# Kernel optimization log

Hardware: AMD Instinct MI355X
Metric: run time of the kernel (lower is better)

## Reference

```python
import jax, jax.numpy as jnp
import numpy as np

N, T, D, H = 128, 128, 1024, 1024


def setup_inputs() -> dict:
    key = jax.random.key(0)
    k_x, k_A, k_wx, k_wh, k_wa = jax.random.split(key, 5)
    x = jax.random.normal(k_x, (N, T, D), dtype=jnp.float32)
    A = jax.random.normal(k_A, (N, H, 4, 4), dtype=jnp.float32)
    Wx = jax.random.normal(k_wx, (D, 4 * H), dtype=jnp.float32) / np.sqrt(D)
    Wh = jax.random.normal(k_wh, (H, 4 * H), dtype=jnp.float32) / np.sqrt(H)
    Wattn = jax.random.normal(k_wa, (H, 4 * H), dtype=jnp.float32) / np.sqrt(H)
    b = jnp.zeros((4 * H,), dtype=jnp.float32)
    return {"x": x, "A": A, "Wx": Wx, "Wh": Wh, "Wattn": Wattn, "b": b}


def reference(x, A, Wx, Wh, Wattn, b):
    n, h_dim = A.shape[0], A.shape[1]
    A_flat = A.reshape(n, h_dim, 16)          # (N, H, 16) spatial flattened
    h0 = A_flat.mean(axis=-1)                 # meanpool over 4x4 grid
    c0 = h0
    scale = 1.0 / np.sqrt(h_dim).astype(np.float32)

    def step(carry, x_t):
        h, c = carry
        # scaled dot-product attention over 16 spatial cells
        attn_w = jax.nn.softmax(jnp.einsum('nh,nhk->nk', h, A_flat) * scale, axis=-1)
        attn = jnp.einsum('nhk,nk->nh', A_flat, attn_w)
        a = x_t @ Wx + h @ Wh + attn @ Wattn + b   # (N, 4H)
        a_i, a_f, a_o, a_g = jnp.split(a, 4, axis=1)
        c_next = jax.nn.sigmoid(a_f) * c + jax.nn.sigmoid(a_i) * jnp.tanh(a_g)
        h_next = jax.nn.sigmoid(a_o) * jnp.tanh(c_next)
        return (h_next, c_next), h_next

    xs = jnp.transpose(x, (1, 0, 2))          # (T, N, D)
    _, hs = jax.lax.scan(step, (h0, c0), xs)  # hs: (T, N, H)
    return jnp.transpose(hs, (1, 0, 2))       # (N, T, H)
```

## Files before the change

### kernel.cpp

```cpp
#include <hip/hip_runtime.h>
#include <math.h>

#define NB 128
#define TT 128
#define HD 1024
#define FH 4096
#define QB 16
#define QSLOT (QB * 2048)

typedef __attribute__((ext_vector_type(8))) short short8v;
typedef __attribute__((ext_vector_type(4))) float float4v;

__device__ __forceinline__ ushort f2b(float f) {
    union { float f; unsigned u; } v; v.f = f;
    unsigned r = (v.u + 0x7fffu + ((v.u >> 16) & 1u)) >> 16;
    return (ushort)r;
}
__device__ __forceinline__ float b2f(ushort u) {
    union { unsigned u; float f; } v; v.u = ((unsigned)u) << 16;
    return v.f;
}
__device__ __forceinline__ float sigm(float x) { return 1.f / (1.f + __expf(-x)); }
__device__ __forceinline__ void gll16(const void* g, void* l) {
    __builtin_amdgcn_global_load_lds(
        (const __attribute__((address_space(1))) void*)g,
        (__attribute__((address_space(3))) void*)l,
        16, 0, 0);
}
__device__ __forceinline__ int swz(int c, int r) {
    return (c & 8) | ((c & 7) ^ (r & 7));
}

__global__ __launch_bounds__(256) void cvt_x(const float* __restrict__ x,
                                             ushort* __restrict__ xb) {
    size_t i = (size_t)blockIdx.x * 256 + threadIdx.x;
    const float4* p = (const float4*)x + i * 2;
    float4 va = p[0], vb = p[1];
    union { ushort u[8]; uint4 v; } o;
    o.u[0] = f2b(va.x); o.u[1] = f2b(va.y); o.u[2] = f2b(va.z); o.u[3] = f2b(va.w);
    o.u[4] = f2b(vb.x); o.u[5] = f2b(vb.y); o.u[6] = f2b(vb.z); o.u[7] = f2b(vb.w);
    ((uint4*)xb)[i] = o.v;
}

__global__ __launch_bounds__(256) void build_wt(const float* __restrict__ Wx,
                                                const float* __restrict__ Wh,
                                                const float* __restrict__ Wattn,
                                                ushort* __restrict__ WT) {
    __shared__ ushort Ls[64][65];
    int k0 = blockIdx.x * 64, n0 = blockIdx.y * 64;
    const float* W; int m;
    if (k0 < 1024)      { W = Wx;    m = 0; }
    else if (k0 < 2048) { W = Wh;    m = 1; }
    else                { W = Wattn; m = 2; }
    const int kk0 = k0 - m * 1024;
    ushort* dstm = WT + (size_t)m * FH * 1024;
    int t = threadIdx.x;
    int cc = t & 63, r4 = t >> 6;
#pragma unroll
    for (int i = 0; i < 16; ++i) {
        int r = i * 4 + r4;
        Ls[r][cc] = f2b(W[(size_t)(kk0 + r) * FH + n0 + cc]);
    }
    __syncthreads();
#pragma unroll
    for (int i = 0; i < 16; ++i) {
        int nn = i * 4 + r4;
        dstm[(size_t)(n0 + nn) * 1024 + kk0 + cc] = Ls[cc][nn];
    }
}

__global__ __launch_bounds__(256) void init_kernel(
    const float* __restrict__ Aflat, float* __restrict__ cbuf,
    ushort* __restrict__ h0buf, ushort* __restrict__ Ab16,
    float* __restrict__ qk0, float* __restrict__ qk1)
{
    __shared__ float red[4][16];
    const int n = blockIdx.x, tid = threadIdx.x;
    const int wv = tid >> 6, l = tid & 63;
    float p[16];
#pragma unroll
    for (int k = 0; k < 16; ++k) p[k] = 0.f;
#pragma unroll
    for (int u = 0; u < 4; ++u) {
        const int h = tid + u * 256;
        const size_t idx = (size_t)n * 1024 + h;
        const float4* a4 = (const float4*)(Aflat + idx * 16);
        float ar[16];
#pragma unroll
        for (int q = 0; q < 4; ++q) {
            float4 v = a4[q];
            ar[q*4+0]=v.x; ar[q*4+1]=v.y; ar[q*4+2]=v.z; ar[q*4+3]=v.w;
        }
        union { ushort us[16]; uint4 v[2]; } ob;
#pragma unroll
        for (int k = 0; k < 16; ++k) ob.us[k] = f2b(ar[k]);
        uint4* dst = (uint4*)(Ab16 + idx * 16);
        dst[0] = ob.v[0]; dst[1] = ob.v[1];

        float s = 0.f;
#pragma unroll
        for (int k = 0; k < 16; ++k) s += ar[k];
        float hv = s * 0.0625f;
        cbuf[idx] = hv;
        h0buf[idx] = f2b(hv);
#pragma unroll
        for (int k = 0; k < 16; ++k) p[k] += hv * ar[k];
    }
#pragma unroll
    for (int k = 0; k < 16; ++k) {
        float v = p[k];
        v += __shfl_xor(v, 32); v += __shfl_xor(v, 16); v += __shfl_xor(v, 8);
        v += __shfl_xor(v, 4);  v += __shfl_xor(v, 2);  v += __shfl_xor(v, 1);
        p[k] = v;
    }
    if (l == 0) {
#pragma unroll
        for (int k = 0; k < 16; ++k) red[wv][k] = p[k];
    }
    __syncthreads();
    if (tid < 16) {
        float val = red[0][tid] + red[1][tid] + red[2][tid] + red[3][tid];
#pragma unroll
        for (int bkt = 0; bkt < QB; ++bkt) {
            qk0[bkt * 2048 + n * 16 + tid] = (bkt == 0) ? val : 0.f;
            qk1[bkt * 2048 + n * 16 + tid] = 0.f;
        }
    }
}

__global__ __launch_bounds__(256) void p_gemm(
    const ushort* __restrict__ Ab16,
    const ushort* __restrict__ WatT,
    ushort* __restrict__ P2)
{
    __shared__ ushort ALDS[4 * 16 * 72];
    __shared__ ushort Bs[256 * 64];
    const int tid = threadIdx.x;
    const int wv = tid >> 6, l = tid & 63;
    const int lr = l & 15, g = l >> 4;
    const int jt = blockIdx.x, n0 = blockIdx.y * 4;
    const int snn = tid >> 6, shl = tid & 63;

    float4v acc[4][4];
#pragma unroll
    for (int i = 0; i < 4; ++i)
#pragma unroll
        for (int j = 0; j < 4; ++j) acc[i][j] = (float4v){0.f, 0.f, 0.f, 0.f};

#pragma unroll 1
    for (int kc = 0; kc < 16; ++kc) {
        __syncthreads();
        {
            const ushort* src = Ab16 + ((size_t)(n0 + snn) * 1024 + kc * 64 + shl) * 16;
            union { uint4 v[2]; ushort us[16]; } iv;
            iv.v[0] = *(const uint4*)src;
            iv.v[1] = *(const uint4*)(src + 8);
#pragma unroll
            for (int k = 0; k < 16; ++k)
                ALDS[(snn * 16 + k) * 72 + shl] = iv.us[k];
        }
#pragma unroll
        for (int i = 0; i < 8; ++i) {
            int s = i * 256 + tid;
            int r = s >> 3, c = (s & 7) ^ (r & 7);
            gll16(WatT + (size_t)(jt * 256 + r) * 1024 + kc * 64 + c * 8,
                  &Bs[s * 8]);
        }
        __syncthreads();
#pragma unroll
        for (int sub = 0; sub < 2; ++sub) {
            short8v af[4], bf[4];
#pragma unroll
            for (int nn = 0; nn < 4; ++nn)
                af[nn] = *(const short8v*)&ALDS[(nn * 16 + lr) * 72 + sub * 32 + g * 8];
#pragma unroll
            for (int nf = 0; nf < 4; ++nf) {
                int rb = wv * 64 + nf * 16 + lr;
                bf[nf] = *(const short8v*)&Bs[rb * 64 + (((sub * 4 + g) ^ (rb & 7)) * 8)];
            }
#pragma unroll
            for (int nn = 0; nn < 4; ++nn)
#pragma unroll
                for (int nf = 0; nf < 4; ++nf)
                    acc[nn][nf] = __builtin_amdgcn_mfma_f32_16x16x32_bf16(
                        af[nn], bf[nf], acc[nn][nf], 0, 0, 0);
        }
    }

#pragma unroll
    for (int nn = 0; nn < 4; ++nn)
#pragma unroll
        for (int nf = 0; nf < 4; ++nf) {
            const int j = jt * 256 + wv * 64 + nf * 16 + lr;
            union { ushort u[4]; uint2 v; } o;
#pragma unroll
            for (int jj = 0; jj < 4; ++jj) o.u[jj] = f2b(acc[nn][nf][jj]);
            *(uint2*)&P2[((size_t)(n0 + nn) * FH + j) * 16 + g * 4] = o.v;
        }
}

__global__ __launch_bounds__(256) void step_kernel(
    const ushort* __restrict__ hcur,
    ushort* __restrict__ hnext,
    const ushort* __restrict__ xb_t,
    const ushort* __restrict__ WxT,
    const ushort* __restrict__ WhT,
    const ushort* __restrict__ P2,
    const ushort* __restrict__ Ab16,
    const float* __restrict__ bias,
    float* __restrict__ cbuf,
    const float* __restrict__ qk_cur,
    float* __restrict__ qk_next,
    float* __restrict__ qk_zero,
    float* __restrict__ out_t)
{
    __shared__ ushort AS[16384];
    __shared__ ushort BS[16384];
    __shared__ float accL[2 * 32 * 33];
    __shared__ float wLDS[32 * 16];

    const int tid = threadIdx.x;
    const int w = tid >> 6, l = tid & 63;
    const int mh = w & 1, kh = w >> 1;
    const int lr = l & 15, g = l >> 4;

    const int bid = blockIdx.x;
    const int xcd = bid & 7, ii = bid >> 3;
    const int bx = xcd * 16 + (ii & 15);
    const int my = ii >> 4;
    const int n0 = my * 32;

    if (bid < 128) qk_zero[bid * 256 + tid] = 0.f;

    if (tid < 32) {
        const float* q = qk_cur + (n0 + tid) * 16;
        float4 s4[4];
#pragma unroll
        for (int q4 = 0; q4 < 4; ++q4) s4[q4] = ((const float4*)q)[q4];
#pragma unroll
        for (int bkt = 1; bkt < QB; ++bkt) {
            const float4* qb = (const float4*)(q + bkt * 2048);
#pragma unroll
            for (int q4 = 0; q4 < 4; ++q4) {
                float4 v = qb[q4];
                s4[q4].x += v.x; s4[q4].y += v.y; s4[q4].z += v.z; s4[q4].w += v.w;
            }
        }
        float s[16];
#pragma unroll
        for (int q4 = 0; q4 < 4; ++q4) {
            s[q4*4+0] = s4[q4].x; s[q4*4+1] = s4[q4].y;
            s[q4*4+2] = s4[q4].z; s[q4*4+3] = s4[q4].w;
        }
        float m = -1e30f;
#pragma unroll
        for (int k = 0; k < 16; ++k) { s[k] *= 0.03125f; m = fmaxf(m, s[k]); }
        float sum = 0.f;
#pragma unroll
        for (int k = 0; k < 16; ++k) { s[k] = __expf(s[k] - m); sum += s[k]; }
        float inv = 1.f / sum;
#pragma unroll
        for (int k = 0; k < 16; ++k) wLDS[tid * 16 + k] = s[k] * inv;
    }

#define STAGE(b, kc)                                                           \
    do {                                                                       \
        _Pragma("unroll")                                                      \
        for (int i = 0; i < 4; ++i) {                                          \
            int u = i * 256 + tid;                                             \
            int skh = u >> 9, rem = u & 511;                                   \
            int r = rem >> 4, c = rem & 15;                                    \
            int lc = swz(c, r);                                                \
            const ushort* src = skh                                            \
                ? hcur + (size_t)(n0 + r) * 1024 + (kc) * 128 + lc * 8         \
                : xb_t + (size_t)(n0 + r) * (TT * HD) + (kc) * 128 + lc * 8;   \
            gll16(src, AS + (((b) * 2 + skh) * 512 + rem) * 8);                \
        }                                                                      \
        _Pragma("unroll")                                                      \
        for (int i = 0; i < 4; ++i) {                                          \
            int u = i * 256 + tid;                                             \
            int skh = u >> 9, rem = u & 511;                                   \
            int r = rem >> 4, c = rem & 15;                                    \
            int lc = swz(c, r);                                                \
            int jg = (r >> 3) * 1024 + bx * 8 + (r & 7);                       \
            const ushort* src = (skh ? WhT : WxT) + (size_t)jg * 1024          \
                                + (kc) * 128 + lc * 8;                         \
            gll16(src, BS + (((b) * 2 + skh) * 512 + rem) * 8);                \
        }                                                                      \
    } while (0)

    float4v acc[2];
    acc[0] = (float4v){0.f, 0.f, 0.f, 0.f};
    acc[1] = (float4v){0.f, 0.f, 0.f, 0.f};

    STAGE(0, 0);
    __syncthreads();
    int buf = 0;
#pragma unroll 1
    for (int kc = 0; kc < 8; ++kc) {
        if (kc < 7) STAGE(buf ^ 1, kc + 1);
        const int base = (buf * 2 + kh) * 512;
        const int ra = mh * 16 + lr;
#pragma unroll
        for (int ks = 0; ks < 4; ++ks) {
            const int c = ks * 4 + g;
            short8v af = *(const short8v*)&AS[(base + ra * 16 + swz(c, ra)) * 8];
#pragma unroll
            for (int nf = 0; nf < 2; ++nf) {
                const int rb = nf * 16 + lr;
                short8v bf = *(const short8v*)&BS[(base + rb * 16 + swz(c, rb)) * 8];
                acc[nf] = __builtin_amdgcn_mfma_f32_16x16x32_bf16(af, bf, acc[nf], 0, 0, 0);
            }
        }
        __syncthreads();
        buf ^= 1;
    }
#undef STAGE

#pragma unroll
    for (int nf = 0; nf < 2; ++nf)
#pragma unroll
        for (int jj = 0; jj < 4; ++jj)
            accL[(kh * 32 + mh * 16 + g * 4 + jj) * 33 + nf * 16 + lr] = acc[nf][jj];
    __syncthreads();

    const int n_l = tid >> 3, hcl = tid & 7;
    const int n = n0 + n_l;
    const int hc = bx * 8 + hcl;

    float wv_[16];
#pragma unroll
    for (int k = 0; k < 16; ++k) wv_[k] = wLDS[n_l * 16 + k];

    float val[4];
#pragma unroll
    for (int q = 0; q < 4; ++q) {
        const int cq = q * 8 + hcl;
        float v = accL[n_l * 33 + cq] + accL[(32 + n_l) * 33 + cq]
                + bias[q * 1024 + hc];
        const ushort* pp = P2 + ((size_t)n * FH + q * 1024 + hc) * 16;
        union { uint4 v[2]; ushort us[16]; } pv;
        pv.v[0] = *(const uint4*)pp;
        pv.v[1] = *(const uint4*)(pp + 8);
#pragma unroll
        for (int k = 0; k < 16; ++k) v += wv_[k] * b2f(pv.us[k]);
        val[q] = v;
    }

    const size_t chidx = (size_t)n * 1024 + hc;
    float cn = sigm(val[1]) * cbuf[chidx] + sigm(val[0]) * tanhf(val[3]);
    float hv = sigm(val[2]) * tanhf(cn);
    cbuf[chidx] = cn;
    out_t[(size_t)n * (TT * HD) + hc] = hv;
    hnext[chidx] = f2b(hv);

    union { uint4 v[2]; ushort us[16]; } av;
    {
        const ushort* ap = Ab16 + chidx * 16;
        av.v[0] = *(const uint4*)ap;
        av.v[1] = *(const uint4*)(ap + 8);
    }
    float vv[16];
#pragma unroll
    for (int k = 0; k < 16; ++k) vv[k] = hv * b2f(av.us[k]);
    {
        bool hi = (hcl & 1);
#pragma unroll
        for (int q = 0; q < 8; ++q) {
            float send = hi ? vv[q] : vv[q + 8];
            float recv = __shfl_xor(send, 1);
            vv[q] = (hi ? vv[q + 8] : vv[q]) + recv;
        }
        hi = (hcl & 2);
#pragma unroll
        for (int q = 0; q < 4; ++q) {
            float send = hi ? vv[q] : vv[q + 4];
            float recv = __shfl_xor(send, 2);
            vv[q] = (hi ? vv[q + 4] : vv[q]) + recv;
        }
        hi = (hcl & 4);
#pragma unroll
        for (int q = 0; q < 2; ++q) {
            float send = hi ? vv[q] : vv[q + 2];
            float recv = __shfl_xor(send, 4);
            vv[q] = (hi ? vv[q + 2] : vv[q]) + recv;
        }
    }
    const int kbase = ((hcl & 1) << 3) | ((hcl & 2) << 1) | ((hcl & 4) >> 1);
    float* qdst = qk_next + (bx & (QB - 1)) * 2048 + n * 16;
    atomicAdd(qdst + kbase,     vv[0]);
    atomicAdd(qdst + kbase + 1, vv[1]);
}

extern "C" void kernel_launch(void* const* d_in, const int* in_sizes, int n_in,
                              void* d_out, int out_size, void* d_ws, size_t ws_size,
                              hipStream_t stream) {
    const float* x     = (const float*)d_in[0];
    const float* A     = (const float*)d_in[1];
    const float* Wx    = (const float*)d_in[2];
    const float* Wh    = (const float*)d_in[3];
    const float* Wattn = (const float*)d_in[4];
    const float* b     = (const float*)d_in[5];
    float* out = (float*)d_out;

    ushort* WT   = (ushort*)d_ws;
    ushort* WxT  = WT;
    ushort* WhT  = WT + (size_t)FH * 1024;
    ushort* WatT = WT + (size_t)2 * FH * 1024;
    ushort* xb   = WT + (size_t)3 * FH * 1024;
    ushort* Ab16 = xb + (size_t)NB * TT * HD;
    ushort* hb   = Ab16 + (size_t)NB * HD * 16;
    float*  cb   = (float*)(hb + (size_t)2 * NB * HD);
    float*  qk   = cb + (size_t)NB * HD;
    ushort* P2   = (ushort*)(qk + 3 * QSLOT);

    cvt_x<<<8192, 256, 0, stream>>>(x, xb);
    build_wt<<<dim3(48, 64), 256, 0, stream>>>(Wx, Wh, Wattn, WT);
    init_kernel<<<NB, 256, 0, stream>>>(A, cb, hb, Ab16, qk, qk + QSLOT);
    p_gemm<<<dim3(16, 32), 256, 0, stream>>>(Ab16, WatT, P2);

    for (int t = 0; t < TT; ++t) {
        const ushort* hc = hb + (size_t)(t & 1) * NB * HD;
        ushort* hn       = hb + (size_t)((t + 1) & 1) * NB * HD;
        const float* qc  = qk + (size_t)(t % 3) * QSLOT;
        float* qn        = qk + (size_t)((t + 1) % 3) * QSLOT;
        float* qz        = qk + (size_t)((t + 2) % 3) * QSLOT;
        step_kernel<<<512, 256, 0, stream>>>(
            hc, hn, xb + (size_t)t * HD, WxT, WhT, P2, Ab16, b, cb,
            qc, qn, qz, out + (size_t)t * HD);
    }
}
```

Baseline: 2.046 ms.

## Precompute x@Wx for all timesteps in one batched GEMM before recurrence

Adds a large bf16 GEMM that computes the input projection x_t@Wx for every timestep up front and stores it in workspace. Each recurrent step kernel then only multiplies by Wh (half the K dimension) and adds the precomputed projection in the epilogue. This takes the x-projection off the sequential critical path and replaces the per-step Wx streaming with one efficient large GEMM. The cost is a 128MB workspace buffer and an extra bf16 rounding of the projection. A fallback path is kept for when the workspace is too small.

```diff
diff --git a/kernel.cpp b/kernel.cpp
--- a/kernel.cpp
+++ b/kernel.cpp
@@ -199,10 +199,109 @@
         }
 }
 
+__global__ __launch_bounds__(256) void xa_gemm2(
+    const float* __restrict__ x,
+    const ushort* __restrict__ WxT,
+    ushort* __restrict__ xab)
+{
+    __shared__ ushort As[2][128 * 64];
+    __shared__ ushort Bs[2][128 * 64];
+    const int tid = threadIdx.x;
+    const int w = tid >> 6, l = tid & 63;
+    const int wm = w >> 1, wn = w & 1;
+    const int lr = l & 15, g = l >> 4;
+    const int n0 = blockIdx.x * 128;
+    const int mt = blockIdx.y;
+    const float* Ax = x + (size_t)mt * 128 * 1024;
+    const ushort* Bb = WxT + (size_t)n0 * 1024;
+
+#define STAGEA(b, kf)                                                          \
+    do {                                                                       \
+        _Pragma("unroll")                                                      \
+        for (int i = 0; i < 4; ++i) {                                          \
+            int u = i * 256 + tid;                                             \
+            int r = u >> 3, c = u & 7;                                         \
+            const float* s = Ax + (size_t)r * 1024 + (kf) + c * 8;             \
+            float4 v0 = *(const float4*)s;                                     \
+            float4 v1 = *(const float4*)(s + 4);                               \
+            union { ushort us[8]; uint4 v; } o;                                \
+            o.us[0]=f2b(v0.x); o.us[1]=f2b(v0.y); o.us[2]=f2b(v0.z);           \
+            o.us[3]=f2b(v0.w); o.us[4]=f2b(v1.x); o.us[5]=f2b(v1.y);           \
+            o.us[6]=f2b(v1.z); o.us[7]=f2b(v1.w);                              \
+            *(uint4*)&As[b][(r * 8 + (c ^ (r & 7))) * 8] = o.v;                \
+        }                                                                      \
+    } while (0)
+#define STAGEB(b, kf)                                                          \
+    do {                                                                       \
+        _Pragma("unroll")                                                      \
+        for (int i = 0; i < 4; ++i) {                                          \
+            int s = i * 256 + tid;                                             \
+            int r = s >> 3, c = s & 7;                                         \
+            gll16(Bb + (size_t)r * 1024 + (kf) + (c ^ (r & 7)) * 8,            \
+                  &Bs[b][s * 8]);                                              \
+        }                                                                      \
+    } while (0)
+
+    float4v acc[4][4];
+#pragma unroll
+    for (int i = 0; i < 4; ++i)
+#pragma unroll
+        for (int j = 0; j < 4; ++j) acc[i][j] = (float4v){0.f, 0.f, 0.f, 0.f};
+
+    STAGEA(0, 0);
+    STAGEB(0, 0);
+    __syncthreads();
+    int buf = 0;
+#pragma unroll 1
+    for (int kc = 0; kc < 16; ++kc) {
+        if (kc < 15) { STAGEA(buf ^ 1, (kc + 1) * 64); STAGEB(buf ^ 1, (kc + 1) * 64); }
+        const ushort* Ab = As[buf];
+        const ushort* Bbuf = Bs[buf];
+#pragma unroll
+        for (int sub = 0; sub < 2; ++sub) {
+            short8v af[4], bf[4];
+#pragma unroll
+            for (int mf = 0; mf < 4; ++mf) {
+                int ra = wm * 64 + mf * 16 + lr;
+                af[mf] = *(const short8v*)&Ab[ra * 64 + (((sub * 4 + g) ^ (ra & 7)) * 8)];
+            }
+#pragma unroll
+            for (int nf = 0; nf < 4; ++nf) {
+                int rb = wn * 64 + nf * 16 + lr;
+                bf[nf] = *(const short8v*)&Bbuf[rb * 64 + (((sub * 4 + g) ^ (rb & 7)) * 8)];
+            }
+#pragma unroll
+            for (int mf = 0; mf < 4; ++mf)
+#pragma unroll
+                for (int nf = 0; nf < 4; ++nf)
+                    acc[mf][nf] = __builtin_amdgcn_mfma_f32_16x16x32_bf16(
+                        af[mf], bf[nf], acc[mf][nf], 0, 0, 0);
+        }
+        __syncthreads();
+        buf ^= 1;
+    }
+#undef STAGEA
+#undef STAGEB
+
+#pragma unroll
+    for (int mf = 0; mf < 4; ++mf)
+#pragma unroll
+        for (int nf = 0; nf < 4; ++nf) {
+            const int col = n0 + wn * 64 + nf * 16 + lr;
+#pragma unroll
+            for (int j = 0; j < 4; ++j) {
+                const int rl = wm * 64 + mf * 16 + g * 4 + j;
+                xab[((size_t)rl * NB + mt) * FH + col] = f2b(acc[mf][nf][j]);
+            }
+        }
+}
+
+template <int XAF>
 __global__ __launch_bounds__(256) void step_kernel(
     const ushort* __restrict__ hcur,
     ushort* __restrict__ hnext,
     const ushort* __restrict__ xb_t,
+    const ushort* __restrict__ xab_t,
     const ushort* __restrict__ WxT,
     const ushort* __restrict__ WhT,
     const ushort* __restrict__ P2,
@@ -271,9 +370,14 @@
             int skh = u >> 9, rem = u & 511;                                   \
             int r = rem >> 4, c = rem & 15;                                    \
             int lc = swz(c, r);                                                \
-            const ushort* src = skh                                            \
-                ? hcur + (size_t)(n0 + r) * 1024 + (kc) * 128 + lc * 8         \
-                : xb_t + (size_t)(n0 + r) * (TT * HD) + (kc) * 128 + lc * 8;   \
+            const ushort* src;                                                 \
+            if (XAF == 1)                                                      \
+                src = hcur + (size_t)(n0 + r) * 1024 + skh * 512               \
+                      + (kc) * 128 + lc * 8;                                   \
+            else                                                               \
+                src = skh                                                      \
+                    ? hcur + (size_t)(n0 + r) * 1024 + (kc) * 128 + lc * 8     \
+                    : xb_t + (size_t)(n0 + r) * (TT * HD) + (kc) * 128 + lc * 8;\
             gll16(src, AS + (((b) * 2 + skh) * 512 + rem) * 8);                \
         }                                                                      \
         _Pragma("unroll")                                                      \
@@ -283,8 +387,12 @@
             int r = rem >> 4, c = rem & 15;                                    \
             int lc = swz(c, r);                                                \
             int jg = (r >> 3) * 1024 + bx * 8 + (r & 7);                       \
-            const ushort* src = (skh ? WhT : WxT) + (size_t)jg * 1024          \
-                                + (kc) * 128 + lc * 8;                         \
+            const ushort* src;                                                 \
+            if (XAF == 1)                                                      \
+                src = WhT + (size_t)jg * 1024 + skh * 512 + (kc) * 128 + lc * 8;\
+            else                                                               \
+                src = (skh ? WhT : WxT) + (size_t)jg * 1024                    \
+                      + (kc) * 128 + lc * 8;                                   \
             gll16(src, BS + (((b) * 2 + skh) * 512 + rem) * 8);                \
         }                                                                      \
     } while (0)
@@ -293,12 +401,13 @@
     acc[0] = (float4v){0.f, 0.f, 0.f, 0.f};
     acc[1] = (float4v){0.f, 0.f, 0.f, 0.f};
 
+    const int NK = (XAF == 1) ? 4 : 8;
     STAGE(0, 0);
     __syncthreads();
     int buf = 0;
 #pragma unroll 1
-    for (int kc = 0; kc < 8; ++kc) {
-        if (kc < 7) STAGE(buf ^ 1, kc + 1);
+    for (int kc = 0; kc < NK; ++kc) {
+        if (kc + 1 < NK) STAGE(buf ^ 1, kc + 1);
         const int base = (buf * 2 + kh) * 512;
         const int ra = mh * 16 + lr;
 #pragma unroll
@@ -338,6 +447,7 @@
         const int cq = q * 8 + hcl;
         float v = accL[n_l * 33 + cq] + accL[(32 + n_l) * 33 + cq]
                 + bias[q * 1024 + hc];
+        if (XAF == 1) v += b2f(xab_t[(size_t)n * FH + q * 1024 + hc]);
         const ushort* pp = P2 + ((size_t)n * FH + q * 1024 + hc) * 16;
         union { uint4 v[2]; ushort us[16]; } pv;
         pv.v[0] = *(const uint4*)pp;
@@ -407,26 +517,46 @@
     ushort* WxT  = WT;
     ushort* WhT  = WT + (size_t)FH * 1024;
     ushort* WatT = WT + (size_t)2 * FH * 1024;
-    ushort* xb   = WT + (size_t)3 * FH * 1024;
-    ushort* Ab16 = xb + (size_t)NB * TT * HD;
+    ushort* Ab16 = WT + (size_t)3 * FH * 1024;
     ushort* hb   = Ab16 + (size_t)NB * HD * 16;
     float*  cb   = (float*)(hb + (size_t)2 * NB * HD);
     float*  qk   = cb + (size_t)NB * HD;
     ushort* P2   = (ushort*)(qk + 3 * QSLOT);
-
-    cvt_x<<<8192, 256, 0, stream>>>(x, xb);
+    ushort* tail = P2 + (size_t)NB * FH * 16;
+
+    const size_t base  = (size_t)((char*)tail - (char*)d_ws);
+    const size_t xasz  = (size_t)TT * NB * FH * 2;
+    const size_t xbsz  = (size_t)NB * TT * HD * 2;
+
     build_wt<<<dim3(48, 64), 256, 0, stream>>>(Wx, Wh, Wattn, WT);
     init_kernel<<<NB, 256, 0, stream>>>(A, cb, hb, Ab16, qk, qk + QSLOT);
     p_gemm<<<dim3(16, 32), 256, 0, stream>>>(Ab16, WatT, P2);
 
-    for (int t = 0; t < TT; ++t) {
-        const ushort* hc = hb + (size_t)(t & 1) * NB * HD;
-        ushort* hn       = hb + (size_t)((t + 1) & 1) * NB * HD;
-        const float* qc  = qk + (size_t)(t % 3) * QSLOT;
-        float* qn        = qk + (size_t)((t + 1) % 3) * QSLOT;
-        float* qz        = qk + (size_t)((t + 2) % 3) * QSLOT;
-        step_kernel<<<512, 256, 0, stream>>>(
-            hc, hn, xb + (size_t)t * HD, WxT, WhT, P2, Ab16, b, cb,
-            qc, qn, qz, out + (size_t)t * HD);
-    }
-}
+    if (ws_size >= base + xasz) {
+        ushort* xab = tail;
+        xa_gemm2<<<dim3(32, 128), 256, 0, stream>>>(x, WxT, xab);
+        for (int t = 0; t < TT; ++t) {
+            const ushort* hc = hb + (size_t)(t & 1) * NB * HD;
+            ushort* hn       = hb + (size_t)((t + 1) & 1) * NB * HD;
+            const float* qc  = qk + (size_t)(t % 3) * QSLOT;
+            float* qn        = qk + (size_t)((t + 1) % 3) * QSLOT;
+            float* qz        = qk + (size_t)((t + 2) % 3) * QSLOT;
+            step_kernel<1><<<512, 256, 0, stream>>>(
+                hc, hn, nullptr, xab + (size_t)t * NB * FH, WxT, WhT, P2, Ab16,
+                b, cb, qc, qn, qz, out + (size_t)t * HD);
+        }
+    } else {
+        ushort* xb = tail;
+        cvt_x<<<8192, 256, 0, stream>>>(x, xb);
+        for (int t = 0; t < TT; ++t) {
+            const ushort* hc = hb + (size_t)(t & 1) * NB * HD;
+            ushort* hn       = hb + (size_t)((t + 1) & 1) * NB * HD;
+            const float* qc  = qk + (size_t)(t % 3) * QSLOT;
+            float* qn        = qk + (size_t)((t + 1) % 3) * QSLOT;
+            float* qz        = qk + (size_t)((t + 2) % 3) * QSLOT;
+            step_kernel<0><<<512, 256, 0, stream>>>(
+                hc, hn, xb + (size_t)t * HD, nullptr, WxT, WhT, P2, Ab16,
+                b, cb, qc, qn, qz, out + (size_t)t * HD);
+        }
+    }
+}
```

New measurement: 1.737 ms. 15.1% less time.
